# Kernel tuning notes

Hardware: AMD Instinct MI355X
Metric: run time of the kernel (lower is better)

Reference implementation:

```python
import jax, jax.numpy as jnp
import numpy as np

S, B, H, V, U = 512, 16, 256, 10000, 10000
LAMBDA_T = 0.1   # flashback default temporal decay
LAMBDA_S = 100.0 # flashback default spatial decay
DAY = 86400.0


def setup_inputs() -> dict:
    key = jax.random.key(0)
    ks = jax.random.split(key, 16)
    x = jax.random.randint(ks[0], (S, B), 0, V)
    t = jax.random.uniform(ks[1], (S, B), jnp.float32) * (7.0 * DAY)  # timestamps in seconds
    s = jax.random.normal(ks[2], (S, B, 2), jnp.float32)              # lat/lon-like coords
    y_t = jax.random.uniform(ks[3], (S, B), jnp.float32)
    y_s = jax.random.normal(ks[4], (S, B, 2), jnp.float32)
    h = jnp.zeros((2, B, H), jnp.float32)
    active_user = jax.random.randint(ks[5], (1, B), 0, U)
    sc = 0.02
    enc_emb = jax.random.normal(ks[6], (V, H), jnp.float32) * sc
    user_emb = jax.random.normal(ks[7], (U, H), jnp.float32) * sc
    Wih_f = jax.random.normal(ks[8], (H, H), jnp.float32) * sc
    Whh_f = jax.random.normal(ks[9], (H, H), jnp.float32) * sc
    b_f = jnp.zeros((H,), jnp.float32)
    Wih_b = jax.random.normal(ks[10], (H, H), jnp.float32) * sc
    Whh_b = jax.random.normal(ks[11], (H, H), jnp.float32) * sc
    b_b = jnp.zeros((H,), jnp.float32)
    fc_W = jax.random.normal(ks[12], (V, 3 * H), jnp.float32) * sc
    fc_b = jnp.zeros((V,), jnp.float32)
    return dict(x=x, t=t, s=s, y_t=y_t, y_s=y_s, h=h, active_user=active_user,
                enc_emb=enc_emb, user_emb=user_emb,
                Wih_f=Wih_f, Whh_f=Whh_f, b_f=b_f,
                Wih_b=Wih_b, Whh_b=Whh_b, b_b=b_b,
                fc_W=fc_W, fc_b=fc_b)


def _rnn_dir(xe, h0, Wih, Whh, b):
    # vanilla tanh RNN over leading (time) axis; xe: [S,B,H]
    def step(hprev, xt):
        hn = jnp.tanh(xt @ Wih.T + hprev @ Whh.T + b)
        return hn, hn
    hT, ys = jax.lax.scan(step, h0, xe)
    return ys, hT


def _forward(x, t, s, h, active_user, enc_emb, user_emb,
             Wih_f, Whh_f, b_f, Wih_b, Whh_b, b_b, fc_W, fc_b):
    seq_len, user_len = x.shape
    x_emb = enc_emb[x]                           # [S,B,H]
    out_f, h_f = _rnn_dir(x_emb, h[0], Wih_f, Whh_f, b_f)
    out_b_rev, h_b = _rnn_dir(x_emb[::-1], h[1], Wih_b, Whh_b, b_b)
    h_out = jnp.stack([h_f, h_b], 0)             # [2,B,H]

    # pairwise causal decay weights (i = query step, j = key step, j <= i)
    dt = t[:, None, :] - t[None, :, :]           # [S,S,B]
    ds = jnp.sqrt(jnp.sum((s[:, None] - s[None, :]) ** 2, axis=-1))  # [S,S,B]
    a = ((jnp.cos(dt * (2.0 * np.pi / DAY)) + 1.0) * 0.5) * jnp.exp(-(dt / DAY) * LAMBDA_T)
    b_w = jnp.exp(-ds * LAMBDA_S)
    w = a * b_w + 1e-10                          # [S,S,B]
    causal = jnp.tril(jnp.ones((seq_len, seq_len), w.dtype))
    w = w * causal[:, :, None]
    sum_w = jnp.sum(w, axis=1)                   # [S,B]
    out_w_forward = jnp.einsum('ijb,jbh->ibh', w, out_f) / sum_w[:, :, None]
    # NOTE: original code has a bug (accumulates out_w_backward into itself),
    # so out_w_backward is identically zero; reproduce faithfully.
    out_w_backward = jnp.zeros_like(out_w_forward)

    out_w = jnp.concatenate([out_w_forward, out_w_backward], axis=2)  # [S,B,2H]
    ow = jnp.transpose(out_w, (1, 0, 2))         # [B,S,2H]
    # dropout is identity in eval mode -> query == out_w
    scores = jnp.einsum('bqd,bkd->bqk', ow, ow) / jnp.sqrt(jnp.asarray(2 * H, ow.dtype))
    alpha = jax.nn.softmax(scores, axis=-1)
    ctx = jnp.einsum('bqk,bkd->bqd', alpha, ow)  # [B,S,2H]
    attn_output = jnp.transpose(ctx, (1, 0, 2))  # [S,B,2H]

    p_u = user_emb[active_user.reshape(user_len)]            # [B,H]
    p_u_b = jnp.broadcast_to(p_u[None], (seq_len, user_len, H))
    out_pu = jnp.concatenate([attn_output, p_u_b], axis=2)   # [S,B,3H]
    y_linear = out_pu @ fc_W.T + fc_b                        # [S,B,V]
    return y_linear, h_out


def reference(x, t, s, y_t, y_s, h, active_user, enc_emb, user_emb,
              Wih_f, Whh_f, b_f, Wih_b, Whh_b, b_b, fc_W, fc_b):
    return _forward(x, t, s, h, active_user, enc_emb, user_emb,
                    Wih_f, Whh_f, b_f, Wih_b, Whh_b, b_b, fc_W, fc_b)
```

## Files before the change

### kernel.cpp

```cpp
#include <hip/hip_runtime.h>

typedef unsigned short ushort_t;
typedef __attribute__((ext_vector_type(8))) short short8;
typedef __attribute__((ext_vector_type(4))) float f32x4;

#define S_LEN 512
#define NB 16
#define NH 256
#define NV 10000

__device__ __forceinline__ unsigned short f2bf(float f){
  unsigned u = __float_as_uint(f);
  u += 0x7fffu + ((u >> 16) & 1u);
  return (unsigned short)(u >> 16);
}


__global__ __launch_bounds__(256) void k_prep_xemb(const int* __restrict__ x,
    const float* __restrict__ emb, ushort_t* __restrict__ xe, ushort_t* __restrict__ xer){
  int g = blockIdx.x * 256 + threadIdx.x;
  int m = g >> 5, c = (g & 31) << 3;
  int xm = x[m];
  const float* src = emb + (size_t)xm * NH + c;
  float4 a = *(const float4*)src, b = *(const float4*)(src + 4);
  union { ushort_t us[8]; uint4 v; } u;
  u.us[0]=f2bf(a.x); u.us[1]=f2bf(a.y); u.us[2]=f2bf(a.z); u.us[3]=f2bf(a.w);
  u.us[4]=f2bf(b.x); u.us[5]=f2bf(b.y); u.us[6]=f2bf(b.z); u.us[7]=f2bf(b.w);
  int s = m >> 4, bidx = m & 15;
  int mr = ((S_LEN - 1 - s) << 4) | bidx;
  *(uint4*)&xe [(size_t)m  * NH + c] = u.v;
  *(uint4*)&xer[(size_t)mr * NH + c] = u.v;
}

__global__ __launch_bounds__(256) void k_cvt(const float* __restrict__ src,
                                             ushort_t* __restrict__ dst, int n){
  int g = (blockIdx.x * 256 + threadIdx.x) * 8;
  if (g >= n) return;
  float4 a = *(const float4*)(src + g), b = *(const float4*)(src + g + 4);
  union { ushort_t us[8]; uint4 v; } u;
  u.us[0]=f2bf(a.x); u.us[1]=f2bf(a.y); u.us[2]=f2bf(a.z); u.us[3]=f2bf(a.w);
  u.us[4]=f2bf(b.x); u.us[5]=f2bf(b.y); u.us[6]=f2bf(b.z); u.us[7]=f2bf(b.w);
  *(uint4*)&dst[g] = u.v;
}

__global__ __launch_bounds__(256) void k_prep_fcw(const float* __restrict__ fcW,
                                                  ushort_t* __restrict__ out){
  int g = blockIdx.x * 256 + threadIdx.x;
  int v = g >> 5, c = (g & 31) << 3;
  union { ushort_t us[8]; uint4 q; } u;
  if (v < NV){
    const float* p = fcW + (size_t)v * 768 + c;
    float4 a = *(const float4*)p, b = *(const float4*)(p + 4);
    u.us[0]=f2bf(a.x); u.us[1]=f2bf(a.y); u.us[2]=f2bf(a.z); u.us[3]=f2bf(a.w);
    u.us[4]=f2bf(b.x); u.us[5]=f2bf(b.y); u.us[6]=f2bf(b.z); u.us[7]=f2bf(b.w);
  } else {
    u.q = make_uint4(0,0,0,0);
  }
  *(uint4*)&out[(size_t)v * NH + c] = u.q;
}

__global__ __launch_bounds__(256) void k_prep_tsT(const float* __restrict__ t,
    const float* __restrict__ s2, float* __restrict__ tT,
    float* __restrict__ sxT, float* __restrict__ syT){
  int g = blockIdx.x * 256 + threadIdx.x;
  int j = g >> 4, b = g & 15;
  tT [b * S_LEN + j] = t[g];
  sxT[b * S_LEN + j] = s2[(size_t)g * 2];
  syT[b * S_LEN + j] = s2[(size_t)g * 2 + 1];
}

__global__ __launch_bounds__(256) void k_prep_w(const float* __restrict__ tT,
    const float* __restrict__ sxT, const float* __restrict__ syT,
    ushort_t* __restrict__ wb, float* __restrict__ rsum){
  int i = blockIdx.x, b = blockIdx.y, tid = threadIdx.x;
  const float C1 = 7.272205216643040e-05f;
  const float C2 = -1.1574074074074074e-06f;
  float ti = tT[b*S_LEN+i], sxi = sxT[b*S_LEN+i], syi = syT[b*S_LEN+i];
  __shared__ float red[256];
  float psum = 0.f;
  #pragma unroll
  for (int u2 = 0; u2 < 2; u2++){
    int j = tid + u2 * 256;
    float w = 0.f;
    if (j <= i){
      float dt = ti - tT[b*S_LEN+j];
      float dx = sxi - sxT[b*S_LEN+j], dy = syi - syT[b*S_LEN+j];
      float ds = sqrtf(dx*dx + dy*dy);
      float a = (__cosf(dt * C1) + 1.f) * 0.5f * __expf(dt * C2);
      float bw = __expf(-100.f * ds);
      w = a * bw + 1e-10f;
    }
    psum += w;
    wb[((size_t)b * S_LEN + i) * S_LEN + j] = f2bf(w);
  }
  red[tid] = psum; __syncthreads();
  for (int st = 128; st > 0; st >>= 1){
    if (tid < st) red[tid] += red[tid + st];
    __syncthreads();
  }
  if (tid == 0) rsum[b * S_LEN + i] = 1.f / red[0];
}

__global__ __launch_bounds__(256) void k_ulog(const int* __restrict__ au,
    const float* __restrict__ uemb, const float* __restrict__ fcW,
    const float* __restrict__ fcb, float* __restrict__ ulog){
  __shared__ float pl[16 * 256];
  int tid = threadIdx.x;
  for (int idx = tid; idx < 16 * 256; idx += 256){
    int b = idx >> 8, hc = idx & 255;
    pl[idx] = uemb[(size_t)au[b] * NH + hc];
  }
  __syncthreads();
  int v = blockIdx.x * 256 + tid;
  if (v >= NV) return;
  float acc[16];
  #pragma unroll
  for (int b = 0; b < 16; b++) acc[b] = 0.f;
  const float* wrow = fcW + (size_t)v * 768 + 512;
  for (int hc = 0; hc < 256; hc += 4){
    float4 w4 = *(const float4*)(wrow + hc);
    #pragma unroll
    for (int b = 0; b < 16; b++){
      acc[b] += w4.x * pl[b*256+hc] + w4.y * pl[b*256+hc+1]
              + w4.z * pl[b*256+hc+2] + w4.w * pl[b*256+hc+3];
    }
  }
  float fb = fcb[v];
  #pragma unroll
  for (int b = 0; b < 16; b++) ulog[(size_t)b * NV + v] = acc[b] + fb;
}

__global__ __launch_bounds__(256) void k_transpose(const ushort_t* __restrict__ src,
    ushort_t* __restrict__ dst, int R, int C, long long sstride, long long dstride){
  __shared__ ushort_t tile[32][33];
  int z = blockIdx.z;
  int c0 = blockIdx.x * 32, r0 = blockIdx.y * 32;
  int tx = threadIdx.x & 31, ty = threadIdx.x >> 5;
  const ushort_t* Sp = src + (size_t)sstride * z;
  ushort_t* Dp = dst + (size_t)dstride * z;
  #pragma unroll
  for (int i = 0; i < 32; i += 8) tile[ty+i][tx] = Sp[(size_t)(r0+ty+i) * C + c0 + tx];
  __syncthreads();
  #pragma unroll
  for (int i = 0; i < 32; i += 8) Dp[(size_t)(c0+ty+i) * R + r0 + tx] = tile[tx][ty+i];
}

__global__ __launch_bounds__(256, 2) void k_gemm(
    const ushort_t* __restrict__ A, const ushort_t* __restrict__ Bt, void* __restrict__ Cp,
    int M, int N, int K, int lda, int ldb, int ldc,
    long long sAz, long long sBz, long long sCz,
    const float* __restrict__ bias,
    const float* __restrict__ rowscale, int rsStride,
    const float* __restrict__ addrow, int ldu,
    float cscale, int cmode){
  __shared__ __align__(16) ushort_t As[128 * 40];
  __shared__ __align__(16) ushort_t Bs[128 * 40];
  int z = blockIdx.z;
  int n0 = blockIdx.x * 128, m0 = blockIdx.y * 128;
  int tid = threadIdx.x;
  int wave = tid >> 6, lane = tid & 63;
  int l15 = lane & 15, q4 = lane >> 4;
  int wm = (wave >> 1) * 64, wn = (wave & 1) * 64;
  const ushort_t* Ab = A + (size_t)sAz * z;
  const ushort_t* Bb = Bt + (size_t)sBz * z;
  int srow = tid >> 1, scol = (tid & 1) * 16;
  f32x4 acc[4][4];
  #pragma unroll
  for (int tm = 0; tm < 4; tm++)
    #pragma unroll
    for (int tn = 0; tn < 4; tn++) acc[tm][tn] = (f32x4){0.f,0.f,0.f,0.f};

  for (int k0 = 0; k0 < K; k0 += 32){
    __syncthreads();
    const ushort_t* ap = Ab + (size_t)(m0+srow)*lda + k0 + scol;
    const ushort_t* bp = Bb + (size_t)(n0+srow)*ldb + k0 + scol;
    *(uint4*)&As[srow*40 + scol]     = *(const uint4*)ap;
    *(uint4*)&As[srow*40 + scol + 8] = *(const uint4*)(ap + 8);
    *(uint4*)&Bs[srow*40 + scol]     = *(const uint4*)bp;
    *(uint4*)&Bs[srow*40 + scol + 8] = *(const uint4*)(bp + 8);
    __syncthreads();
    short8 af[4], bf[4];
    #pragma unroll
    for (int tm = 0; tm < 4; tm++) af[tm] = *(const short8*)&As[(wm + tm*16 + l15)*40 + q4*8];
    #pragma unroll
    for (int tn = 0; tn < 4; tn++) bf[tn] = *(const short8*)&Bs[(wn + tn*16 + l15)*40 + q4*8];
    #pragma unroll
    for (int tm = 0; tm < 4; tm++)
      #pragma unroll
      for (int tn = 0; tn < 4; tn++)
        acc[tm][tn] = __builtin_amdgcn_mfma_f32_16x16x32_bf16(af[tm], bf[tn], acc[tm][tn], 0, 0, 0);
  }

  #pragma unroll
  for (int tm = 0; tm < 4; tm++)
    #pragma unroll
    for (int tn = 0; tn < 4; tn++)
      #pragma unroll
      for (int r = 0; r < 4; r++){
        int mr = m0 + wm + tm*16 + q4*4 + r;
        int nc = n0 + wn + tn*16 + l15;
        if (nc < N){
          float v = acc[tm][tn][r] * cscale;
          if (bias)     v += bias[nc];
          if (rowscale) v *= rowscale[(size_t)z * rsStride + mr];
          if (addrow)   v += addrow[(size_t)(mr & 15) * ldu + nc];
          if (cmode == 0){
            ((float*)Cp)[(size_t)sCz * z + (size_t)mr * ldc + nc] = v;
          } else if (cmode == 1){
            ((ushort_t*)Cp)[(size_t)sCz * z + (size_t)mr * ldc + nc] = f2bf(v);
          } else {
            ((ushort_t*)Cp)[((size_t)mr * 16 + z) * ldc + nc] = f2bf(v);
          }
        }
      }
}

__global__ __launch_bounds__(256, 1) void k_rnn(
    const float* __restrict__ WhhF, const float* __restrict__ WhhB,
    const float* __restrict__ xWf, const float* __restrict__ xWb,
    const float* __restrict__ h0,
    ushort_t* __restrict__ outf,
    float* __restrict__ hout){
  int dir = blockIdx.x >> 1, half = blockIdx.x & 1;
  const float* Whh = dir ? WhhB : WhhF;
  const float* xW  = dir ? xWb : xWf;
  int tid = threadIdx.x, wave = tid >> 6, lane = tid & 63;
  int l15 = lane & 15, q4 = lane >> 4;
  __shared__ __align__(16) ushort_t hl[2][8 * 264];

  for (int idx = tid; idx < 2048; idx += 256){
    int m = idx >> 8, n = idx & 255;
    hl[0][m*264 + n] = f2bf(h0[((size_t)dir * 16 + half * 8 + m) * NH + n]);
  }

  short8 bfr[4][8];
  #pragma unroll
  for (int tn = 0; tn < 4; tn++)
    #pragma unroll
    for (int kk = 0; kk < 8; kk++){
      int n = wave*64 + tn*16 + l15;
      int k = kk*32 + q4*8;
      const float* wp = Whh + (size_t)n * NH + k;
      float4 wa = *(const float4*)wp, wb2 = *(const float4*)(wp + 4);
      short8 f;
      f[0]=(short)f2bf(wa.x); f[1]=(short)f2bf(wa.y); f[2]=(short)f2bf(wa.z); f[3]=(short)f2bf(wa.w);
      f[4]=(short)f2bf(wb2.x); f[5]=(short)f2bf(wb2.y); f[6]=(short)f2bf(wb2.z); f[7]=(short)f2bf(wb2.w);
      bfr[tn][kk] = f;
    }

  int hiTn  = q4 >> 1;
  int mb    = (q4 & 1) * 4;
  int ncol0 = wave*64 + hiTn*32 + l15;

  float xwE[8], xwO[8];
  #pragma unroll
  for (int r = 0; r < 4; r++){
    xwE[r]   = xW[(size_t)(half*8 + mb + r) * NH + ncol0];
    xwE[4+r] = xW[(size_t)(half*8 + mb + r) * NH + ncol0 + 16];
    xwO[r]   = xW[(size_t)(16 + half*8 + mb + r) * NH + ncol0];
    xwO[4+r] = xW[(size_t)(16 + half*8 + mb + r) * NH + ncol0 + 16];
  }
  __syncthreads();

#define RNN_STEP(S_, RB_, WB_, XWU_)                                              \
  {                                                                               \
    short8 af[8];                                                                 \
    _Pragma("unroll")                                                             \
    for (int kk = 0; kk < 8; kk++)                                                \
      af[kk] = *(const short8*)&hl[RB_][(lane & 7)*264 + kk*32 + q4*8];           \
    f32x4 acc0 = (f32x4){0.f,0.f,0.f,0.f}, acc1 = acc0, acc2 = acc0, acc3 = acc0; \
    _Pragma("unroll")                                                             \
    for (int kk = 0; kk < 8; kk++){                                               \
      acc0 = __builtin_amdgcn_mfma_f32_16x16x32_bf16(af[kk], bfr[0][kk], acc0, 0,0,0); \
      acc1 = __builtin_amdgcn_mfma_f32_16x16x32_bf16(af[kk], bfr[1][kk], acc1, 0,0,0); \
      acc2 = __builtin_amdgcn_mfma_f32_16x16x32_bf16(af[kk], bfr[2][kk], acc2, 0,0,0); \
      acc3 = __builtin_amdgcn_mfma_f32_16x16x32_bf16(af[kk], bfr[3][kk], acc3, 0,0,0); \
    }                                                                             \
    f32x4 accA = hiTn ? acc2 : acc0;                                              \
    f32x4 accB = hiTn ? acc3 : acc1;                                              \
    _Pragma("unroll")                                                             \
    for (int r = 0; r < 4; r++){                                                  \
      float pre0 = accA[r] + XWU_[r];                                             \
      float pre1 = accB[r] + XWU_[4+r];                                           \
      float ex0 = __expf(2.f * pre0), ex1 = __expf(2.f * pre1);                   \
      float hv0 = 1.f - 2.f * __builtin_amdgcn_rcpf(ex0 + 1.f);                   \
      float hv1 = 1.f - 2.f * __builtin_amdgcn_rcpf(ex1 + 1.f);                   \
      int m = mb + r;                                                             \
      ushort_t hb0 = f2bf(hv0), hb1 = f2bf(hv1);                                  \
      hl[WB_][m*264 + ncol0]      = hb0;                                          \
      hl[WB_][m*264 + ncol0 + 16] = hb1;                                          \
      if (dir == 0){                                                              \
        outf[((size_t)(half*8+m) * 512 + (S_)) * NH + ncol0]      = hb0;          \
        outf[((size_t)(half*8+m) * 512 + (S_)) * NH + ncol0 + 16] = hb1;          \
      }                                                                           \
      if ((S_) == 511){                                                           \
        hout[((size_t)dir*16 + half*8 + m) * NH + ncol0]      = hv0;              \
        hout[((size_t)dir*16 + half*8 + m) * NH + ncol0 + 16] = hv1;              \
      }                                                                           \
    }                                                                             \
    if ((S_) < 510){                                                              \
      _Pragma("unroll")                                                           \
      for (int r = 0; r < 4; r++){                                                \
        XWU_[r]   = xW[((size_t)((S_)+2)*16 + half*8 + mb + r) * NH + ncol0];     \
        XWU_[4+r] = xW[((size_t)((S_)+2)*16 + half*8 + mb + r) * NH + ncol0 + 16];\
      }                                                                           \
    }                                                                             \
    asm volatile("s_waitcnt lgkmcnt(0)" ::: "memory");                            \
    __builtin_amdgcn_s_barrier();                                                 \
    asm volatile("" ::: "memory");                                                \
  }

  for (int s = 0; s < 512; s += 2){
    RNN_STEP(s,     0, 1, xwE)
    RNN_STEP(s + 1, 1, 0, xwO)
  }
#undef RNN_STEP
}

__global__ __launch_bounds__(256) void k_softmax(const float* __restrict__ sc,
                                                 ushort_t* __restrict__ alpha){
  int q = blockIdx.x, z = blockIdx.y, tid = threadIdx.x;
  const float* row = sc + ((size_t)z * S_LEN + q) * S_LEN;
  float v0 = row[tid], v1 = row[tid + 256];
  __shared__ float red[256];
  red[tid] = fmaxf(v0, v1); __syncthreads();
  for (int st = 128; st > 0; st >>= 1){
    if (tid < st) red[tid] = fmaxf(red[tid], red[tid + st]);
    __syncthreads();
  }
  float mx = red[0]; __syncthreads();
  float e0 = __expf(v0 - mx), e1 = __expf(v1 - mx);
  red[tid] = e0 + e1; __syncthreads();
  for (int st = 128; st > 0; st >>= 1){
    if (tid < st) red[tid] += red[tid + st];
    __syncthreads();
  }
  float inv = 1.f / red[0];
  ushort_t* arow = alpha + ((size_t)z * S_LEN + q) * S_LEN;
  arow[tid]       = f2bf(e0 * inv);
  arow[tid + 256] = f2bf(e1 * inv);
}

extern "C" void kernel_launch(void* const* d_in, const int* in_sizes, int n_in,
                              void* d_out, int out_size, void* d_ws, size_t ws_size,
                              hipStream_t stream){
  const int*   x    = (const int*)d_in[0];
  const float* t    = (const float*)d_in[1];
  const float* s2   = (const float*)d_in[2];
  const float* h0   = (const float*)d_in[5];
  const int*   au   = (const int*)d_in[6];
  const float* emb  = (const float*)d_in[7];
  const float* uemb = (const float*)d_in[8];
  const float* WihF = (const float*)d_in[9];
  const float* WhhF = (const float*)d_in[10];
  const float* bF   = (const float*)d_in[11];
  const float* WihB = (const float*)d_in[12];
  const float* WhhB = (const float*)d_in[13];
  const float* bB   = (const float*)d_in[14];
  const float* fcW  = (const float*)d_in[15];
  const float* fcb  = (const float*)d_in[16];
  float* y    = (float*)d_out;
  float* hout = y + (size_t)S_LEN * NB * NV;

  char* wsc = (char*)d_ws;
  size_t off = 0;
  auto alloc = [&](size_t bytes) -> void* {
    void* p = wsc + off;
    off += (bytes + 255) & ~(size_t)255;
    return p;
  };
  ushort_t* xe    = (ushort_t*)alloc(8192 * 256 * 2);
  ushort_t* xer   = (ushort_t*)alloc(8192 * 256 * 2);
  ushort_t* wihf  = (ushort_t*)alloc(256 * 256 * 2);
  ushort_t* wihb  = (ushort_t*)alloc(256 * 256 * 2);
  float*    xwf   = (float*)alloc((size_t)8192 * 256 * 4);
  float*    xwb   = (float*)alloc((size_t)8192 * 256 * 4);
  ushort_t* outf  = (ushort_t*)alloc((size_t)16 * 512 * 256 * 2);
  ushort_t* outfT = (ushort_t*)alloc((size_t)16 * 256 * 512 * 2);
  ushort_t* wbuf  = (ushort_t*)alloc((size_t)16 * 512 * 512 * 2);
  float*    rsum  = (float*)alloc(16 * 512 * 4);
  ushort_t* owf   = (ushort_t*)alloc((size_t)16 * 512 * 256 * 2);
  ushort_t* owfT  = (ushort_t*)alloc((size_t)16 * 256 * 512 * 2);
  ushort_t* fcw1  = (ushort_t*)alloc((size_t)10112 * 256 * 2);
  float*    ulog  = (float*)alloc((size_t)16 * NV * 4);
  float*    tT    = (float*)alloc(16 * 512 * 4);
  float*    sxT   = (float*)alloc(16 * 512 * 4);
  float*    syT   = (float*)alloc(16 * 512 * 4);
  ushort_t* ctx   = (ushort_t*)alloc((size_t)8192 * 256 * 2);
  float*    scores = xwf;
  ushort_t* alpha  = wbuf;

  k_prep_xemb<<<dim3(1024), dim3(256), 0, stream>>>(x, emb, xe, xer);
  k_cvt<<<dim3(32), dim3(256), 0, stream>>>(WihF, wihf, 65536);
  k_cvt<<<dim3(32), dim3(256), 0, stream>>>(WihB, wihb, 65536);
  k_prep_fcw<<<dim3(1264), dim3(256), 0, stream>>>(fcW, fcw1);
  k_prep_tsT<<<dim3(32), dim3(256), 0, stream>>>(t, s2, tT, sxT, syT);
  k_prep_w<<<dim3(512, 16), dim3(256), 0, stream>>>(tT, sxT, syT, wbuf, rsum);
  k_ulog<<<dim3(40), dim3(256), 0, stream>>>(au, uemb, fcW, fcb, ulog);

  k_gemm<<<dim3(2, 64, 1), dim3(256), 0, stream>>>(xe, wihf, xwf,
      8192, 256, 256, 256, 256, 256, 0, 0, 0, bF, nullptr, 0, nullptr, 0, 1.f, 0);
  k_gemm<<<dim3(2, 64, 1), dim3(256), 0, stream>>>(xer, wihb, xwb,
      8192, 256, 256, 256, 256, 256, 0, 0, 0, bB, nullptr, 0, nullptr, 0, 1.f, 0);

  k_rnn<<<dim3(4), dim3(256), 0, stream>>>(WhhF, WhhB, xwf, xwb, h0, outf, hout);

  k_transpose<<<dim3(8, 16, 16), dim3(256), 0, stream>>>(outf, outfT, 512, 256,
      (long long)512 * 256, (long long)256 * 512);

  k_gemm<<<dim3(2, 4, 16), dim3(256), 0, stream>>>(wbuf, outfT, owf,
      512, 256, 512, 512, 512, 256,
      (long long)512 * 512, (long long)256 * 512, (long long)512 * 256,
      nullptr, rsum, 512, nullptr, 0, 1.f, 1);
  k_transpose<<<dim3(8, 16, 16), dim3(256), 0, stream>>>(owf, owfT, 512, 256,
      (long long)512 * 256, (long long)256 * 512);

  k_gemm<<<dim3(4, 4, 16), dim3(256), 0, stream>>>(owf, owf, scores,
      512, 512, 256, 256, 256, 512,
      (long long)512 * 256, (long long)512 * 256, (long long)512 * 512,
      nullptr, nullptr, 0, nullptr, 0, 0.04419417382415922f, 0);

  k_softmax<<<dim3(512, 16), dim3(256), 0, stream>>>(scores, alpha);

  k_gemm<<<dim3(2, 4, 16), dim3(256), 0, stream>>>(alpha, owfT, ctx,
      512, 256, 512, 512, 512, 256,
      (long long)512 * 512, (long long)256 * 512, 0,
      nullptr, nullptr, 0, nullptr, 0, 1.f, 2);

  k_gemm<<<dim3(79, 64, 1), dim3(256), 0, stream>>>(ctx, fcw1, y,
      8192, 10000, 256, 256, 256, 10000, 0, 0, 0,
      nullptr, nullptr, 0, ulog, 10000, 1.f, 0);
}
```

Before: 1.119 ms.

## Split RNN recurrence across 8 waves per block to halve per-wave MFMA chain

The sequential RNN kernel now uses 512 threads (8 waves) per block instead of 4. Each wave owns 32 output columns instead of 64, so it issues 16 MFMAs per step rather than 32 and holds half as many weight fragments in registers. This shortens the serial critical path of each of the 512 steps. Pointer arithmetic for the xW prefetch and the output stores is also turned into incrementing pointers. The cost is a barrier across more waves every step, and duplicated LDS reads of h by each wave.

```diff
diff --git a/kernel.cpp b/kernel.cpp
--- a/kernel.cpp
+++ b/kernel.cpp
@@ -215,7 +215,7 @@
       }
 }
 
-__global__ __launch_bounds__(256, 1) void k_rnn(
+__global__ __launch_bounds__(512, 1) void k_rnn(
     const float* __restrict__ WhhF, const float* __restrict__ WhhB,
     const float* __restrict__ xWf, const float* __restrict__ xWb,
     const float* __restrict__ h0,
@@ -228,17 +228,17 @@
   int l15 = lane & 15, q4 = lane >> 4;
   __shared__ __align__(16) ushort_t hl[2][8 * 264];
 
-  for (int idx = tid; idx < 2048; idx += 256){
+  for (int idx = tid; idx < 2048; idx += 512){
     int m = idx >> 8, n = idx & 255;
     hl[0][m*264 + n] = f2bf(h0[((size_t)dir * 16 + half * 8 + m) * NH + n]);
   }
 
-  short8 bfr[4][8];
-  #pragma unroll
-  for (int tn = 0; tn < 4; tn++)
+  short8 bfr[2][8];
+  #pragma unroll
+  for (int tn = 0; tn < 2; tn++)
     #pragma unroll
     for (int kk = 0; kk < 8; kk++){
-      int n = wave*64 + tn*16 + l15;
+      int n = wave*32 + tn*16 + l15;
       int k = kk*32 + q4*8;
       const float* wp = Whh + (size_t)n * NH + k;
       float4 wa = *(const float4*)wp, wb2 = *(const float4*)(wp + 4);
@@ -248,18 +248,24 @@
       bfr[tn][kk] = f;
     }
 
-  int hiTn  = q4 >> 1;
-  int mb    = (q4 & 1) * 4;
-  int ncol0 = wave*64 + hiTn*32 + l15;
-
-  float xwE[8], xwO[8];
+  int myTn = q4 >> 1;
+  int mb   = (q4 & 1) * 4;
+  int ncol = wave*32 + myTn*16 + l15;
+
+  const float* xwp = xW + (size_t)(half*8 + mb) * NH + ncol;
+  float xwE[4], xwO[4];
   #pragma unroll
   for (int r = 0; r < 4; r++){
-    xwE[r]   = xW[(size_t)(half*8 + mb + r) * NH + ncol0];
-    xwE[4+r] = xW[(size_t)(half*8 + mb + r) * NH + ncol0 + 16];
-    xwO[r]   = xW[(size_t)(16 + half*8 + mb + r) * NH + ncol0];
-    xwO[4+r] = xW[(size_t)(16 + half*8 + mb + r) * NH + ncol0 + 16];
-  }
+    xwE[r] = xwp[r * 256];
+    xwO[r] = xwp[r * 256 + 16 * 256];
+  }
+  xwp += 2 * 16 * 256;
+
+  ushort_t* outp0 = outf + (size_t)(half*8 + mb) * 512 * NH + ncol;
+  ushort_t* outp1 = outp0 + (size_t)512 * NH;
+  ushort_t* outp2 = outp1 + (size_t)512 * NH;
+  ushort_t* outp3 = outp2 + (size_t)512 * NH;
+
   __syncthreads();
 
 #define RNN_STEP(S_, RB_, WB_, XWU_)                                              \
@@ -268,42 +274,35 @@
     _Pragma("unroll")                                                             \
     for (int kk = 0; kk < 8; kk++)                                                \
       af[kk] = *(const short8*)&hl[RB_][(lane & 7)*264 + kk*32 + q4*8];           \
-    f32x4 acc0 = (f32x4){0.f,0.f,0.f,0.f}, acc1 = acc0, acc2 = acc0, acc3 = acc0; \
+    f32x4 acc0 = (f32x4){0.f,0.f,0.f,0.f}, acc1 = acc0;                           \
     _Pragma("unroll")                                                             \
     for (int kk = 0; kk < 8; kk++){                                               \
       acc0 = __builtin_amdgcn_mfma_f32_16x16x32_bf16(af[kk], bfr[0][kk], acc0, 0,0,0); \
       acc1 = __builtin_amdgcn_mfma_f32_16x16x32_bf16(af[kk], bfr[1][kk], acc1, 0,0,0); \
-      acc2 = __builtin_amdgcn_mfma_f32_16x16x32_bf16(af[kk], bfr[2][kk], acc2, 0,0,0); \
-      acc3 = __builtin_amdgcn_mfma_f32_16x16x32_bf16(af[kk], bfr[3][kk], acc3, 0,0,0); \
     }                                                                             \
-    f32x4 accA = hiTn ? acc2 : acc0;                                              \
-    f32x4 accB = hiTn ? acc3 : acc1;                                              \
+    f32x4 accS = myTn ? acc1 : acc0;                                              \
+    float hv[4];                                                                  \
     _Pragma("unroll")                                                             \
     for (int r = 0; r < 4; r++){                                                  \
-      float pre0 = accA[r] + XWU_[r];                                             \
-      float pre1 = accB[r] + XWU_[4+r];                                           \
-      float ex0 = __expf(2.f * pre0), ex1 = __expf(2.f * pre1);                   \
-      float hv0 = 1.f - 2.f * __builtin_amdgcn_rcpf(ex0 + 1.f);                   \
-      float hv1 = 1.f - 2.f * __builtin_amdgcn_rcpf(ex1 + 1.f);                   \
-      int m = mb + r;                                                             \
-      ushort_t hb0 = f2bf(hv0), hb1 = f2bf(hv1);                                  \
-      hl[WB_][m*264 + ncol0]      = hb0;                                          \
-      hl[WB_][m*264 + ncol0 + 16] = hb1;                                          \
-      if (dir == 0){                                                              \
-        outf[((size_t)(half*8+m) * 512 + (S_)) * NH + ncol0]      = hb0;          \
-        outf[((size_t)(half*8+m) * 512 + (S_)) * NH + ncol0 + 16] = hb1;          \
-      }                                                                           \
-      if ((S_) == 511){                                                           \
-        hout[((size_t)dir*16 + half*8 + m) * NH + ncol0]      = hv0;              \
-        hout[((size_t)dir*16 + half*8 + m) * NH + ncol0 + 16] = hv1;              \
-      }                                                                           \
+      float pre = accS[r] + XWU_[r];                                              \
+      float ex = __expf(2.f * pre);                                               \
+      hv[r] = 1.f - 2.f * __builtin_amdgcn_rcpf(ex + 1.f);                        \
+      hl[WB_][(mb + r)*264 + ncol] = f2bf(hv[r]);                                 \
+    }                                                                             \
+    if (dir == 0){                                                                \
+      outp0[0] = f2bf(hv[0]); outp1[0] = f2bf(hv[1]);                             \
+      outp2[0] = f2bf(hv[2]); outp3[0] = f2bf(hv[3]);                             \
+      outp0 += 256; outp1 += 256; outp2 += 256; outp3 += 256;                     \
+    }                                                                             \
+    if ((S_) == 511){                                                             \
+      _Pragma("unroll")                                                           \
+      for (int r = 0; r < 4; r++)                                                 \
+        hout[((size_t)dir*16 + half*8 + mb + r) * NH + ncol] = hv[r];             \
     }                                                                             \
     if ((S_) < 510){                                                              \
       _Pragma("unroll")                                                           \
-      for (int r = 0; r < 4; r++){                                                \
-        XWU_[r]   = xW[((size_t)((S_)+2)*16 + half*8 + mb + r) * NH + ncol0];     \
-        XWU_[4+r] = xW[((size_t)((S_)+2)*16 + half*8 + mb + r) * NH + ncol0 + 16];\
-      }                                                                           \
+      for (int r = 0; r < 4; r++) XWU_[r] = xwp[r * 256];                         \
+      xwp += 16 * 256;                                                            \
     }                                                                             \
     asm volatile("s_waitcnt lgkmcnt(0)" ::: "memory");                            \
     __builtin_amdgcn_s_barrier();                                                 \
@@ -403,7 +402,7 @@
   k_gemm<<<dim3(2, 64, 1), dim3(256), 0, stream>>>(xer, wihb, xwb,
       8192, 256, 256, 256, 256, 256, 0, 0, 0, bB, nullptr, 0, nullptr, 0, 1.f, 0);
 
-  k_rnn<<<dim3(4), dim3(256), 0, stream>>>(WhhF, WhhB, xwf, xwb, h0, outf, hout);
+  k_rnn<<<dim3(4), dim3(512), 0, stream>>>(WhhF, WhhB, xwf, xwb, h0, outf, hout);
 
   k_transpose<<<dim3(8, 16, 16), dim3(256), 0, stream>>>(outf, outfT, 512, 256,
       (long long)512 * 256, (long long)256 * 512);
```

Result: faster. 966.1 us (-13.7%).
